# Optimization experiments

Hardware: AMD Instinct MI355X
Metric: run time of the kernel (lower is better)

The kernel has to match this reference:

```python
import jax, jax.numpy as jnp
import numpy as np

B, H, LQ, LK, D, HID = 2, 1, 512, 512, 64, 128


def setup_inputs() -> dict:
    key = jax.random.key(0)
    ks = jax.random.split(key, 8)
    f = lambda k, shape, s=1.0: jax.random.normal(k, shape, dtype=jnp.float32) * s
    return {
        "q": f(ks[0], (B, H, LQ, D)),
        "k": f(ks[1], (B, H, LK, D)),
        "v": f(ks[2], (B, H, LK, D)),
        "mask": jnp.zeros((B, H, LQ, LK), jnp.float32),
        # shared q/k/v projection (self.w) and output projection (self.dense)
        "Ww": f(ks[3], (D, D), 0.1), "wb": jnp.zeros((D,), jnp.float32),
        "Wd": f(ks[4], (D, D), 0.1), "db": jnp.zeros((D,), jnp.float32),
        # two-layer MLP NN: 2*D -> HID -> 1
        "W1": f(ks[5], (2 * D, HID), 0.1), "b1": jnp.zeros((HID,), jnp.float32),
        "W2": f(ks[6], (HID, 1), 0.1), "b2": jnp.zeros((1,), jnp.float32),
    }


def _sim_scores(q, k, W1, b1, W2, b2, make_sym):
    # Equivalent to tile+concat+MLP, but splits W1 so the 2*D concat tensor
    # is never materialized; only the [B,H,Lq,Lk,HID] hidden is.
    W1q, W1k = W1[:D], W1[D:]
    qa = q @ W1q  # [B,H,Lq,HID]
    kb = k @ W1k  # [B,H,Lk,HID]
    h = jax.nn.relu(qa[:, :, :, None, :] + kb[:, :, None, :, :] + b1)
    s = (h @ W2)[..., 0] + b2[0]  # [B,H,Lq,Lk]
    if make_sym:
        # concat([k, q]) order: hidden2 = relu(k_j @ W1q + q_i @ W1k + b1)
        qb = q @ W1k
        ka = k @ W1q
        h2 = jax.nn.relu(qb[:, :, :, None, :] + ka[:, :, None, :, :] + b1)
        s = s + (h2 @ W2)[..., 0] + b2[0]
    return s


def reference(q, k, v, mask, Ww, wb, Wd, db, W1, b1, W2, b2):
    make_sym = True
    qp = q @ Ww + wb
    kp = k @ Ww + wb
    vp = v @ Ww + wb
    logits = _sim_scores(qp, kp, W1, b1, W2, b2, make_sym)
    logits = logits + mask * (-1e9)
    attn = jax.nn.softmax(logits, axis=-1)  # [B,H,Lq,Lk]
    out = attn @ vp                          # [B,H,Lq,D]
    out = out @ Wd + db
    return (out, attn)
```

## Files before the change

kernel.cpp:

```cpp
#include <hip/hip_runtime.h>
#include <hip/hip_bf16.h>


#define NROWS 1024
#define DD    64
#define HH    128
#define LK_   512
#define QR    4

__global__ __launch_bounds__(128)
void proj_kernel(const float* __restrict__ q, const float* __restrict__ k,
                 const float* __restrict__ v,
                 const float* __restrict__ Ww, const float* __restrict__ wb,
                 const float* __restrict__ W1, const float* __restrict__ b1,
                 float* __restrict__ qp, float* __restrict__ kp, float* __restrict__ vp,
                 float* __restrict__ qa, float* __restrict__ qb,
                 float* __restrict__ ka, float* __restrict__ kb)
{
    const int r    = blockIdx.x;
    const int type = r >> 10;
    const int idx  = r & 1023;
    const int t    = threadIdx.x;

    const float* src = (type == 0) ? q : (type == 1) ? k : v;

    __shared__ float x[DD];
    __shared__ float xp[DD];

    if (t < DD) x[t] = src[idx * DD + t];
    __syncthreads();

    if (t < DD) {
        float acc = wb[t];
        #pragma unroll
        for (int c = 0; c < DD; ++c) acc = fmaf(x[c], Ww[c * DD + t], acc);
        xp[t] = acc;
        float* dst = (type == 0) ? qp : (type == 1) ? kp : vp;
        dst[idx * DD + t] = acc;
    }
    __syncthreads();

    if (type == 2) return;

    float accA = 0.f;
    float accB = 0.f;
    #pragma unroll
    for (int d = 0; d < DD; ++d) {
        const float xv = xp[d];
        accA = fmaf(xv, W1[d * HH + t],        accA);
        accB = fmaf(xv, W1[(DD + d) * HH + t], accB);
    }
    if (type == 0) {
        qa[idx * HH + t] = accA + b1[t];
        qb[idx * HH + t] = accB + b1[t];
    } else {
        ka[idx * HH + t] = accA;
        kb[idx * HH + t] = accB;
    }
}

__global__ __launch_bounds__(256)
void trans_kernel(const float* __restrict__ ka, const float* __restrict__ kb,
                  float4* __restrict__ kaT, float4* __restrict__ kbT)
{
    const int j0 = blockIdx.x * 64;
    const int h0 = blockIdx.y * 64;
    const int b  = blockIdx.z;
    const int tx = threadIdx.x & 63;
    const int ty = threadIdx.x >> 6;

    __shared__ float ta[64][65];
    __shared__ float tb[64][65];

    #pragma unroll
    for (int rr = 0; rr < 16; ++rr) {
        const int jl = ty + rr * 4;
        const int g  = (b * LK_ + j0 + jl) * HH + h0 + tx;
        ta[jl][tx] = ka[g];
        tb[jl][tx] = kb[g];
    }
    __syncthreads();
    #pragma unroll
    for (int rr = 0; rr < 4; ++rr) {
        const int hq  = ty + rr * 4;
        const int h4g = blockIdx.y * 16 + hq;
        const int hl  = hq * 4;
        const int o   = (b * (HH / 4) + h4g) * LK_ + j0 + tx;
        kaT[o] = make_float4(ta[tx][hl+0], ta[tx][hl+1], ta[tx][hl+2], ta[tx][hl+3]);
        kbT[o] = make_float4(tb[tx][hl+0], tb[tx][hl+1], tb[tx][hl+2], tb[tx][hl+3]);
    }
}

__global__ __launch_bounds__(512)
void attn_kernel(const float* __restrict__ mask,
                 const float* __restrict__ vp,
                 const float* __restrict__ qa, const float* __restrict__ qb,
                 const float4* __restrict__ kaT, const float4* __restrict__ kbT,
                 const float* __restrict__ W2, const float* __restrict__ b2,
                 const float* __restrict__ Wd, const float* __restrict__ db,
                 float* __restrict__ out, float* __restrict__ attn)
{
    const int row0 = blockIdx.x * QR;
    const int b    = row0 >> 9;
    const int t    = threadIdx.x;
    const int wid  = t >> 6;
    const int lane = t & 63;
    const int j    = t;

    __shared__ float p_int[LK_ * QR];
    __shared__ float redm[8][QR];
    __shared__ float reds[8][QR];
    __shared__ float opart[8][QR][DD];
    __shared__ float o_l[QR][DD];

    const float4* kaTb = kaT + b * (HH / 4) * LK_;
    const float4* kbTb = kbT + b * (HH / 4) * LK_;
    const float4* qa4  = reinterpret_cast<const float4*>(qa + row0 * HH);
    const float4* qb4  = reinterpret_cast<const float4*>(qb + row0 * HH);
    const float4* w24  = reinterpret_cast<const float4*>(W2);

    float mk[QR];
    #pragma unroll
    for (int r = 0; r < QR; ++r) mk[r] = mask[(row0 + r) * LK_ + j];

    float s1[QR] = {0.f, 0.f, 0.f, 0.f};
    float s2[QR] = {0.f, 0.f, 0.f, 0.f};
    #pragma unroll 4
    for (int h4 = 0; h4 < HH / 4; ++h4) {
        const float4 w   = w24[h4];
        const float4 kb4 = kbTb[h4 * LK_ + j];
        const float4 ka4 = kaTb[h4 * LK_ + j];
        #pragma unroll
        for (int r = 0; r < QR; ++r) {
            const float4 A  = qa4[r * (HH / 4) + h4];
            const float4 Bq = qb4[r * (HH / 4) + h4];
            s1[r] = fmaf(fmaxf(A.x  + kb4.x, 0.f), w.x, s1[r]);
            s1[r] = fmaf(fmaxf(A.y  + kb4.y, 0.f), w.y, s1[r]);
            s1[r] = fmaf(fmaxf(A.z  + kb4.z, 0.f), w.z, s1[r]);
            s1[r] = fmaf(fmaxf(A.w  + kb4.w, 0.f), w.w, s1[r]);
            s2[r] = fmaf(fmaxf(Bq.x + ka4.x, 0.f), w.x, s2[r]);
            s2[r] = fmaf(fmaxf(Bq.y + ka4.y, 0.f), w.y, s2[r]);
            s2[r] = fmaf(fmaxf(Bq.z + ka4.z, 0.f), w.z, s2[r]);
            s2[r] = fmaf(fmaxf(Bq.w + ka4.w, 0.f), w.w, s2[r]);
        }
    }

    const float b2v = b2[0];
    float sv[QR];
    #pragma unroll
    for (int r = 0; r < QR; ++r)
        sv[r] = s1[r] + s2[r] + 2.f * b2v + mk[r] * (-1e9f);

    float m[QR];
    #pragma unroll
    for (int r = 0; r < QR; ++r) {
        float mv = sv[r];
        #pragma unroll
        for (int off = 32; off > 0; off >>= 1) mv = fmaxf(mv, __shfl_xor(mv, off));
        if (lane == 0) redm[wid][r] = mv;
    }
    __syncthreads();
    #pragma unroll
    for (int r = 0; r < QR; ++r) {
        float mv = redm[0][r];
        #pragma unroll
        for (int w = 1; w < 8; ++w) mv = fmaxf(mv, redm[w][r]);
        m[r] = mv;
    }

    float e[QR];
    #pragma unroll
    for (int r = 0; r < QR; ++r) {
        e[r] = expf(sv[r] - m[r]);
        float s = e[r];
        #pragma unroll
        for (int off = 32; off > 0; off >>= 1) s += __shfl_xor(s, off);
        if (lane == 0) reds[wid][r] = s;
    }
    __syncthreads();

    float pv[QR];
    #pragma unroll
    for (int r = 0; r < QR; ++r) {
        float s = reds[0][r];
        #pragma unroll
        for (int w = 1; w < 8; ++w) s += reds[w][r];
        pv[r] = e[r] / s;
        attn[(row0 + r) * LK_ + j] = pv[r];
    }
    *reinterpret_cast<float4*>(&p_int[j * QR]) =
        make_float4(pv[0], pv[1], pv[2], pv[3]);
    __syncthreads();

    float acc[QR] = {0.f, 0.f, 0.f, 0.f};
    {
        const int jb = wid * 64;
        const float* vpb = vp + (b * LK_ + jb) * DD;
        #pragma unroll 8
        for (int jj = 0; jj < 64; ++jj) {
            const float4 pj = *reinterpret_cast<const float4*>(&p_int[(jb + jj) * QR]);
            const float vv = vpb[jj * DD + lane];
            acc[0] = fmaf(pj.x, vv, acc[0]);
            acc[1] = fmaf(pj.y, vv, acc[1]);
            acc[2] = fmaf(pj.z, vv, acc[2]);
            acc[3] = fmaf(pj.w, vv, acc[3]);
        }
    }
    #pragma unroll
    for (int r = 0; r < QR; ++r) opart[wid][r][lane] = acc[r];
    __syncthreads();

    if (t < QR * DD) {
        const int r = t >> 6, d = t & 63;
        float o = opart[0][r][d];
        #pragma unroll
        for (int w = 1; w < 8; ++w) o += opart[w][r][d];
        o_l[r][d] = o;
    }
    __syncthreads();

    if (t < QR * DD) {
        const int r = t >> 6, d = t & 63;
        float res = db[d];
        #pragma unroll
        for (int c = 0; c < DD; ++c) res = fmaf(o_l[r][c], Wd[c * DD + d], res);
        out[(row0 + r) * DD + d] = res;
    }
}

extern "C" void kernel_launch(void* const* d_in, const int* in_sizes, int n_in,
                              void* d_out, int out_size, void* d_ws, size_t ws_size,
                              hipStream_t stream)
{
    const float* q    = (const float*)d_in[0];
    const float* k    = (const float*)d_in[1];
    const float* v    = (const float*)d_in[2];
    const float* mask = (const float*)d_in[3];
    const float* Ww   = (const float*)d_in[4];
    const float* wb   = (const float*)d_in[5];
    const float* Wd   = (const float*)d_in[6];
    const float* db   = (const float*)d_in[7];
    const float* W1   = (const float*)d_in[8];
    const float* b1   = (const float*)d_in[9];
    const float* W2   = (const float*)d_in[10];
    const float* b2   = (const float*)d_in[11];

    float* ws = (float*)d_ws;
    float* qp = ws;
    float* kp = qp + NROWS * DD;
    float* vp = kp + NROWS * DD;
    float* qa = vp + NROWS * DD;
    float* qb = qa + NROWS * HH;
    float* ka = qb + NROWS * HH;
    float* kb = ka + NROWS * HH;
    float4* kaT = (float4*)(kb + NROWS * HH);
    float4* kbT = kaT + 2 * (HH / 4) * LK_;

    float* out  = (float*)d_out;
    float* attn = out + NROWS * DD;

    proj_kernel<<<dim3(3072), dim3(128), 0, stream>>>(
        q, k, v, Ww, wb, W1, b1, qp, kp, vp, qa, qb, ka, kb);

    trans_kernel<<<dim3(8, 2, 2), dim3(256), 0, stream>>>(ka, kb, kaT, kbT);

    attn_kernel<<<dim3(NROWS / QR), dim3(512), 0, stream>>>(
        mask, vp, qa, qb, kaT, kbT, W2, b2, Wd, db, out, attn);
}
```

Baseline: 116.8 us.

## Fuse K transpose into projection kernel and drop unused qp/kp stores

The projection kernel now writes ka/kb directly in the transposed float4-interleaved layout the attention kernel reads, which removes the separate transpose kernel launch and one round trip through global memory. The qp/kp outputs, which nothing reads, are no longer stored. In the attention kernel the qa/qb loads change from float4 to scalar reads and the unroll factor drops from 4 to 2, which may lower register pressure but could add load instructions. The transposed stores from the projection kernel are strided and only partly coalesced.

```diff
diff --git a/kernel.cpp b/kernel.cpp
--- a/kernel.cpp
+++ b/kernel.cpp
@@ -13,9 +13,9 @@
                  const float* __restrict__ v,
                  const float* __restrict__ Ww, const float* __restrict__ wb,
                  const float* __restrict__ W1, const float* __restrict__ b1,
-                 float* __restrict__ qp, float* __restrict__ kp, float* __restrict__ vp,
+                 float* __restrict__ vp,
                  float* __restrict__ qa, float* __restrict__ qb,
-                 float* __restrict__ ka, float* __restrict__ kb)
+                 float* __restrict__ kaTf, float* __restrict__ kbTf)
 {
     const int r    = blockIdx.x;
     const int type = r >> 10;
@@ -35,8 +35,7 @@
         #pragma unroll
         for (int c = 0; c < DD; ++c) acc = fmaf(x[c], Ww[c * DD + t], acc);
         xp[t] = acc;
-        float* dst = (type == 0) ? qp : (type == 1) ? kp : vp;
-        dst[idx * DD + t] = acc;
+        if (type == 2) vp[idx * DD + t] = acc;
     }
     __syncthreads();
 
@@ -54,40 +53,11 @@
         qa[idx * HH + t] = accA + b1[t];
         qb[idx * HH + t] = accB + b1[t];
     } else {
-        ka[idx * HH + t] = accA;
-        kb[idx * HH + t] = accB;
-    }
-}
-
-__global__ __launch_bounds__(256)
-void trans_kernel(const float* __restrict__ ka, const float* __restrict__ kb,
-                  float4* __restrict__ kaT, float4* __restrict__ kbT)
-{
-    const int j0 = blockIdx.x * 64;
-    const int h0 = blockIdx.y * 64;
-    const int b  = blockIdx.z;
-    const int tx = threadIdx.x & 63;
-    const int ty = threadIdx.x >> 6;
-
-    __shared__ float ta[64][65];
-    __shared__ float tb[64][65];
-
-    #pragma unroll
-    for (int rr = 0; rr < 16; ++rr) {
-        const int jl = ty + rr * 4;
-        const int g  = (b * LK_ + j0 + jl) * HH + h0 + tx;
-        ta[jl][tx] = ka[g];
-        tb[jl][tx] = kb[g];
-    }
-    __syncthreads();
-    #pragma unroll
-    for (int rr = 0; rr < 4; ++rr) {
-        const int hq  = ty + rr * 4;
-        const int h4g = blockIdx.y * 16 + hq;
-        const int hl  = hq * 4;
-        const int o   = (b * (HH / 4) + h4g) * LK_ + j0 + tx;
-        kaT[o] = make_float4(ta[tx][hl+0], ta[tx][hl+1], ta[tx][hl+2], ta[tx][hl+3]);
-        kbT[o] = make_float4(tb[tx][hl+0], tb[tx][hl+1], tb[tx][hl+2], tb[tx][hl+3]);
+        const int b  = idx >> 9;
+        const int j  = idx & (LK_ - 1);
+        const int o  = ((b * (HH / 4) + (t >> 2)) * LK_ + j) * 4 + (t & 3);
+        kaTf[o] = accA;
+        kbTf[o] = accB;
     }
 }
 
@@ -115,8 +85,8 @@
 
     const float4* kaTb = kaT + b * (HH / 4) * LK_;
     const float4* kbTb = kbT + b * (HH / 4) * LK_;
-    const float4* qa4  = reinterpret_cast<const float4*>(qa + row0 * HH);
-    const float4* qb4  = reinterpret_cast<const float4*>(qb + row0 * HH);
+    const float*  qaR  = qa + row0 * HH;
+    const float*  qbR  = qb + row0 * HH;
     const float4* w24  = reinterpret_cast<const float4*>(W2);
 
     float mk[QR];
@@ -125,23 +95,22 @@
 
     float s1[QR] = {0.f, 0.f, 0.f, 0.f};
     float s2[QR] = {0.f, 0.f, 0.f, 0.f};
-    #pragma unroll 4
+    #pragma unroll 2
     for (int h4 = 0; h4 < HH / 4; ++h4) {
         const float4 w   = w24[h4];
         const float4 kb4 = kbTb[h4 * LK_ + j];
         const float4 ka4 = kaTb[h4 * LK_ + j];
+        const int h = h4 * 4;
         #pragma unroll
         for (int r = 0; r < QR; ++r) {
-            const float4 A  = qa4[r * (HH / 4) + h4];
-            const float4 Bq = qb4[r * (HH / 4) + h4];
-            s1[r] = fmaf(fmaxf(A.x  + kb4.x, 0.f), w.x, s1[r]);
-            s1[r] = fmaf(fmaxf(A.y  + kb4.y, 0.f), w.y, s1[r]);
-            s1[r] = fmaf(fmaxf(A.z  + kb4.z, 0.f), w.z, s1[r]);
-            s1[r] = fmaf(fmaxf(A.w  + kb4.w, 0.f), w.w, s1[r]);
-            s2[r] = fmaf(fmaxf(Bq.x + ka4.x, 0.f), w.x, s2[r]);
-            s2[r] = fmaf(fmaxf(Bq.y + ka4.y, 0.f), w.y, s2[r]);
-            s2[r] = fmaf(fmaxf(Bq.z + ka4.z, 0.f), w.z, s2[r]);
-            s2[r] = fmaf(fmaxf(Bq.w + ka4.w, 0.f), w.w, s2[r]);
+            s1[r] = fmaf(fmaxf(qaR[r * HH + h + 0] + kb4.x, 0.f), w.x, s1[r]);
+            s1[r] = fmaf(fmaxf(qaR[r * HH + h + 1] + kb4.y, 0.f), w.y, s1[r]);
+            s1[r] = fmaf(fmaxf(qaR[r * HH + h + 2] + kb4.z, 0.f), w.z, s1[r]);
+            s1[r] = fmaf(fmaxf(qaR[r * HH + h + 3] + kb4.w, 0.f), w.w, s1[r]);
+            s2[r] = fmaf(fmaxf(qbR[r * HH + h + 0] + ka4.x, 0.f), w.x, s2[r]);
+            s2[r] = fmaf(fmaxf(qbR[r * HH + h + 1] + ka4.y, 0.f), w.y, s2[r]);
+            s2[r] = fmaf(fmaxf(qbR[r * HH + h + 2] + ka4.z, 0.f), w.z, s2[r]);
+            s2[r] = fmaf(fmaxf(qbR[r * HH + h + 3] + ka4.w, 0.f), w.w, s2[r]);
         }
     }
 
@@ -246,24 +215,19 @@
     const float* b2   = (const float*)d_in[11];
 
     float* ws = (float*)d_ws;
-    float* qp = ws;
-    float* kp = qp + NROWS * DD;
-    float* vp = kp + NROWS * DD;
+    float* vp = ws;
     float* qa = vp + NROWS * DD;
     float* qb = qa + NROWS * HH;
-    float* ka = qb + NROWS * HH;
-    float* kb = ka + NROWS * HH;
-    float4* kaT = (float4*)(kb + NROWS * HH);
-    float4* kbT = kaT + 2 * (HH / 4) * LK_;
+    float* kaTf = qb + NROWS * HH;
+    float* kbTf = kaTf + NROWS * HH;
 
     float* out  = (float*)d_out;
     float* attn = out + NROWS * DD;
 
     proj_kernel<<<dim3(3072), dim3(128), 0, stream>>>(
-        q, k, v, Ww, wb, W1, b1, qp, kp, vp, qa, qb, ka, kb);
-
-    trans_kernel<<<dim3(8, 2, 2), dim3(256), 0, stream>>>(ka, kb, kaT, kbT);
+        q, k, v, Ww, wb, W1, b1, vp, qa, qb, kaTf, kbTf);
 
     attn_kernel<<<dim3(NROWS / QR), dim3(512), 0, stream>>>(
-        mask, vp, qa, qb, kaT, kbT, W2, b2, Wd, db, out, attn);
+        mask, vp, qa, qb, (const float4*)kaTf, (const float4*)kbTf,
+        W2, b2, Wd, db, out, attn);
 }
```

Result: faster. 102.0 us (median of 2 runs) (-12.7%).
